# Kernel optimization log

Hardware: AMD Instinct MI355X
Metric: run time of the kernel (lower is better)

## Reference

```python
import jax, jax.numpy as jnp
import numpy as np

# video grid and attention geometry (must match init_kwargs)
F_T, H_T, W_T = 4, 32, 32
K = 3                      # kernel_size (odd)
P = K // 2
T = F_T * H_T * W_T        # max_num_tokens = 4096
HEADS = 8
DIM_HEAD = 64
SCALE = DIM_HEAD ** -0.5
DIM = 512
INNER = HEADS * DIM_HEAD


def _build_window_indices():
    # flat token index grid, padded with sentinel T (out-of-range -> zero row after gather)
    idx = np.arange(T).reshape(F_T, H_T, W_T)
    padded = np.full((F_T + 2 * P, H_T + 2 * P, W_T + 2 * P), T, dtype=np.int64)
    padded[P:P + F_T, P:P + H_T, P:P + W_T] = idx
    # [T, K^3] neighborhood indices, kernel offsets in (kf, kh, kw) C-order (matches unfoldNd)
    win = np.lib.stride_tricks.sliding_window_view(padded, (K, K, K)).reshape(T, K ** 3)
    # causal: mask keys whose flat index is strictly in the future of the query
    causal = np.arange(T)[:, None] < win
    causal = np.concatenate([np.zeros((T, 1), dtype=bool), causal], axis=1)  # BOS column never masked
    return jnp.asarray(win), jnp.asarray(causal)

WIN_IDX, CAUSAL_MASK = _build_window_indices()


def setup_inputs() -> dict:
    key = jax.random.key(0)
    k0, k1, k2, k3 = jax.random.split(key, 4)
    n = T  # 1 BOS + (T-1) video tokens; padding logic pads body to exactly T tokens
    x = jax.random.normal(k0, (2, n, DIM), dtype=jnp.float32)
    Wq = jax.random.normal(k1, (DIM, INNER), dtype=jnp.float32) * (DIM ** -0.5)
    Wkv = jax.random.normal(k2, (DIM, 2 * INNER), dtype=jnp.float32) * (DIM ** -0.5)
    Wo = jax.random.normal(k3, (INNER, DIM), dtype=jnp.float32) * (INNER ** -0.5)
    bo = jnp.zeros((DIM,), dtype=jnp.float32)
    return {"x": x, "Wq": Wq, "Wkv": Wkv, "Wo": Wo, "bo": bo}


def _split_heads(t, b):
    # [b, n, h*d] -> [(b*h), n, d]
    n = t.shape[1]
    return t.reshape(b, n, HEADS, DIM_HEAD).transpose(0, 2, 1, 3).reshape(b * HEADS, n, DIM_HEAD)


def reference(x, Wq, Wkv, Wo, bo):
    b, n, _ = x.shape
    tpf = H_T * W_T
    padding = tpf - (n - 1) % tpf  # pads body tokens to a multiple of tokens_per_frame
    x = jnp.pad(x, ((0, 0), (0, padding), (0, 0)))
    q = x @ Wq
    k, v = jnp.split(x @ Wkv, 2, axis=-1)
    q, k, v = (_split_heads(t, b) for t in (q, k, v))
    bh = b * HEADS
    q = q[:, 1:] * SCALE            # drop BOS query; [bh, T, d]
    bos_v = v[:, :1]                # BOS attends only to itself -> its value passes through
    k_bos, k = k[:, :1], k[:, 1:]
    v_bos, v = v[:, :1], v[:, 1:]
    # gather K^3 3D neighborhoods; sentinel index T maps to a zero row
    zero_row = jnp.zeros((bh, 1, DIM_HEAD), dtype=k.dtype)
    k_nb = jnp.concatenate([k, zero_row], axis=1)[:, WIN_IDX]   # [bh, T, K^3, d]
    v_nb = jnp.concatenate([v, zero_row], axis=1)[:, WIN_IDX]
    # prepend global BOS key/value to every window
    k_nb = jnp.concatenate([jnp.broadcast_to(k_bos[:, :, None], (bh, T, 1, DIM_HEAD)), k_nb], axis=2)
    v_nb = jnp.concatenate([jnp.broadcast_to(v_bos[:, :, None], (bh, T, 1, DIM_HEAD)), v_nb], axis=2)
    sim = jnp.einsum('bid,bijd->bij', q, k_nb)                  # [bh, T, K^3+1]
    sim = jnp.where(CAUSAL_MASK[None], -jnp.finfo(sim.dtype).max, sim)
    attn = jax.nn.softmax(sim, axis=-1)
    out = jnp.einsum('bij,bijd->bid', attn, v_nb)               # [bh, T, d]
    out = jnp.concatenate([bos_v, out], axis=1)                 # [bh, T+1, d]
    np_tok = out.shape[1]
    out = out.reshape(b, HEADS, np_tok, DIM_HEAD).transpose(0, 2, 1, 3).reshape(b, np_tok, INNER)
    return (out @ Wo + bo)[:, :n]
```

## Files before the change

### kernel.cpp

```cpp
#include <hip/hip_runtime.h>


#define T_TOK   4096
#define BATCH   2
#define MROWS   (BATCH * T_TOK)
#define DIM     512
#define NQKV    1536

typedef unsigned short u16;
typedef unsigned int   u32;
typedef unsigned long long u64;
typedef __attribute__((ext_vector_type(8))) short short8;
typedef __attribute__((ext_vector_type(4))) float f32x4;

__device__ __forceinline__ u16 f2bf(float f) {
    u32 u = __float_as_uint(f);
    return (u16)((u + 0x7fffu + ((u >> 16) & 1u)) >> 16);
}
__device__ __forceinline__ float b2f(u16 u) {
    return __uint_as_float(((u32)u) << 16);
}

__device__ __forceinline__ void gload_lds16(const void* g, void* l) {
    __builtin_amdgcn_global_load_lds(
        (const __attribute__((address_space(1))) void*)g,
        (__attribute__((address_space(3))) void*)l, 16, 0, 0);
}

__global__ void cast_all_kernel(const float4* __restrict__ x,
                                const float* __restrict__ Wq, const float* __restrict__ Wkv,
                                const float* __restrict__ Wo,
                                u16* __restrict__ xb, u16* __restrict__ Wt,
                                u16* __restrict__ Wot) {
    int blk = blockIdx.x;
    if (blk < 4096) {
        int i = blk * 256 + threadIdx.x;
        float4 v = x[i];
        u64 pack = (u64)f2bf(v.x) | ((u64)f2bf(v.y) << 16) |
                   ((u64)f2bf(v.z) << 32) | ((u64)f2bf(v.w) << 48);
        ((u64*)xb)[i] = pack;
    } else {
        int idx = (blk - 4096) * 256 + threadIdx.x;
        if (idx < 786432) {
            int k = idx / 1536, n = idx % 1536;
            float v = (n < 512) ? Wq[k * 512 + n] : Wkv[k * 1024 + (n - 512)];
            Wt[n * 512 + k] = f2bf(v);
        } else {
            int i2 = idx - 786432;
            int k = i2 >> 9, n = i2 & 511;
            Wot[n * 512 + k] = f2bf(Wo[k * 512 + n]);
        }
    }
}

template <int MODE>
__global__ __launch_bounds__(256)
void gemm_nt(const u16* __restrict__ A, const u16* __restrict__ B,
             void* __restrict__ Cv, const float* __restrict__ bias,
             int lda, int ldb, int ldc) {
    constexpr int K = 512, BK = 32;
    __shared__ __align__(16) char lds[16384];
    const int tid  = threadIdx.x;
    const int lane = tid & 63, wave = tid >> 6;
    const int quad = lane >> 4, mrow = lane & 15;
    const int wm = wave >> 1, wn = wave & 1;
    const int bm = blockIdx.y, bn = blockIdx.x;

    const char* gptr[4];
    char*       lptr[4];
    #pragma unroll
    for (int it = 0; it < 4; ++it) {
        int c   = it * 256 + tid;
        int inB = (c >= 512);
        int a   = inB ? c - 512 : c;
        int r   = a >> 2;
        int kc  = ((a & 3) - (r >> 1)) & 3;
        int row = (inB ? bn : bm) * 128 + r;
        const u16* base = inB ? B : A;
        int ld = inB ? ldb : lda;
        gptr[it] = (const char*)(base + (size_t)row * ld + kc * 8);
        lptr[it] = (char*)lds + it * 4096 + wave * 1024;
    }
    const short8* aLds[4];
    const short8* bLds[4];
    #pragma unroll
    for (int i = 0; i < 4; ++i) {
        int ra = wm * 64 + i * 16 + mrow;
        aLds[i] = (const short8*)(lds + (ra * 4 + ((quad + (ra >> 1)) & 3)) * 16);
        int rb = wn * 64 + i * 16 + mrow;
        bLds[i] = (const short8*)(lds + 8192 + (rb * 4 + ((quad + (rb >> 1)) & 3)) * 16);
    }

    f32x4 acc[4][4] = {};
    for (int k0 = 0; k0 < K; k0 += BK) {
        #pragma unroll
        for (int it = 0; it < 4; ++it)
            gload_lds16(gptr[it] + 2 * k0, lptr[it]);
        __syncthreads();
        short8 af[4], bf[4];
        #pragma unroll
        for (int i = 0; i < 4; ++i) { af[i] = *aLds[i]; bf[i] = *bLds[i]; }
        #pragma unroll
        for (int i = 0; i < 4; ++i)
            #pragma unroll
            for (int j = 0; j < 4; ++j)
                acc[i][j] = __builtin_amdgcn_mfma_f32_16x16x32_bf16(af[i], bf[j], acc[i][j], 0, 0, 0);
        __syncthreads();
    }

    #pragma unroll
    for (int i = 0; i < 4; ++i) {
        #pragma unroll
        for (int j = 0; j < 4; ++j) {
            int colg = bn * 128 + wn * 64 + j * 16 + mrow;
            #pragma unroll
            for (int r = 0; r < 4; ++r) {
                int rowg = bm * 128 + wm * 64 + i * 16 + quad * 4 + r;
                if (MODE == 0) {
                    ((u16*)Cv)[(size_t)rowg * ldc + colg] = f2bf(acc[i][j][r]);
                } else {
                    ((float*)Cv)[(size_t)rowg * ldc + colg] = acc[i][j][r] + bias[colg];
                }
            }
        }
    }
}

__global__ __launch_bounds__(256)
void attn_kernel(const u16* __restrict__ QKV, u16* __restrict__ O) {
    const int wid  = blockIdx.x * 4 + (threadIdx.x >> 6);
    const int lane = threadIdx.x & 63;
    const int bh = wid >> 12;
    const int ti = wid & 4095;
    const int b = bh >> 3, h = bh & 7;
    const size_t baseQ = (size_t)b * T_TOK * NQKV;
    const size_t baseO = (size_t)b * T_TOK * DIM;

    if (ti == 0) {
        O[baseO + h * 64 + lane] = QKV[baseQ + 1024 + h * 64 + lane];
        return;
    }
    const int t = ti - 1;
    const int f = t >> 10, hh = (t >> 5) & 31, ww = t & 31;

    const int j = lane >> 2, g = lane & 3;
    int jm1 = j - 1;
    int dh9 = ((jm1 * 11) >> 5) - 1;
    int dw9 = jm1 - (dh9 + 1) * 3 - 1;
    int df = (j >= 1 && j <= 9) ? -1 : 0;
    int dh = (j >= 1 && j <= 9) ? dh9 : ((j >= 10 && j <= 12) ? -1 : 0);
    int dw = (j >= 1 && j <= 9) ? dw9 :
             ((j >= 10 && j <= 12) ? (j - 11) : ((j == 13) ? -1 : 0));
    int nf = f + df, nh = hh + dh, nw = ww + dw;
    int valid = (nf >= 0) && ((unsigned)nh < 32u) && ((unsigned)nw < 32u)
                && (j >= 1) && (j <= 14);
    int p = valid ? (t + 1 + df * 1024 + dh * 32 + dw) : 0;
    int score_on = valid || (j == 0);

    const u16* qrow = QKV + baseQ + (size_t)(t + 1) * NQKV + h * 64 + g * 16;
    short8 q0 = *(const short8*)qrow;
    short8 q1 = *(const short8*)(qrow + 8);
    const u16* krow = QKV + baseQ + (size_t)p * NQKV + 512 + h * 64 + g * 16;
    short8 k0 = *(const short8*)krow;
    short8 k1 = *(const short8*)(krow + 8);
    float s = 0.f;
    #pragma unroll
    for (int i = 0; i < 8; ++i) {
        s += b2f((u16)q0[i]) * b2f((u16)k0[i]);
        s += b2f((u16)q1[i]) * b2f((u16)k1[i]);
    }
    s += __shfl_xor(s, 1);
    s += __shfl_xor(s, 2);
    s *= 0.125f;
    s = score_on ? s : -3.0e38f;

    float m = s;
    #pragma unroll
    for (int off = 4; off <= 32; off <<= 1) m = fmaxf(m, __shfl_xor(m, off));
    float pe = __expf(s - m);
    float l = pe;
    #pragma unroll
    for (int off = 4; off <= 32; off <<= 1) l += __shfl_xor(l, off);

    float acc = 0.f;
    const u16* vbase = QKV + baseQ + 1024 + h * 64 + lane;
    #pragma unroll
    for (int jj = 0; jj < 15; ++jj) {
        int   ps = __builtin_amdgcn_readlane(p, jj * 4);
        float pj = __uint_as_float(
                     (u32)__builtin_amdgcn_readlane((int)__float_as_uint(pe), jj * 4));
        float vv = b2f(vbase[(size_t)ps * NQKV]);
        acc += pj * vv;
    }
    O[baseO + (size_t)ti * DIM + h * 64 + lane] = f2bf(acc * __frcp_rn(l));
}

extern "C" void kernel_launch(void* const* d_in, const int* in_sizes, int n_in,
                              void* d_out, int out_size, void* d_ws, size_t ws_size,
                              hipStream_t stream) {
    const float* x   = (const float*)d_in[0];
    const float* Wq  = (const float*)d_in[1];
    const float* Wkv = (const float*)d_in[2];
    const float* Wo  = (const float*)d_in[3];
    const float* bo  = (const float*)d_in[4];
    float* out = (float*)d_out;
    char* ws = (char*)d_ws;

    u16* xb  = (u16*)(ws + 0);
    u16* Wt  = (u16*)(ws + 8388608);
    u16* Wot = (u16*)(ws + 9961472);
    u16* QKV = (u16*)(ws + 10485760);
    u16* O   = (u16*)(ws + 0);

    cast_all_kernel<<<dim3(8192), dim3(256), 0, stream>>>(
        (const float4*)x, Wq, Wkv, Wo, xb, Wt, Wot);
    gemm_nt<0><<<dim3(12, 64), dim3(256), 0, stream>>>(xb, Wt, (void*)QKV, nullptr, 512, 512, 1536);
    attn_kernel<<<dim3(16384), dim3(256), 0, stream>>>(QKV, O);
    gemm_nt<1><<<dim3(4, 64), dim3(256), 0, stream>>>(O, Wot, (void*)out, bo, 512, 512, 512);
}
```

Baseline: 142.2 us.

## Tile weight transposes through LDS, retile output GEMM, streamline attention gather

Result: slower. 147.9 us (+4.0%).

```diff
diff --git a/kernel.cpp b/kernel.cpp
--- a/kernel.cpp
+++ b/kernel.cpp
@@ -2,8 +2,6 @@
 
 
 #define T_TOK   4096
-#define BATCH   2
-#define MROWS   (BATCH * T_TOK)
 #define DIM     512
 #define NQKV    1536
 
@@ -32,90 +30,112 @@
                                 const float* __restrict__ Wo,
                                 u16* __restrict__ xb, u16* __restrict__ Wt,
                                 u16* __restrict__ Wot) {
+    __shared__ float S[64 * 65];
     int blk = blockIdx.x;
+    int tid = threadIdx.x;
     if (blk < 4096) {
-        int i = blk * 256 + threadIdx.x;
+        int i = blk * 256 + tid;
         float4 v = x[i];
         u64 pack = (u64)f2bf(v.x) | ((u64)f2bf(v.y) << 16) |
                    ((u64)f2bf(v.z) << 32) | ((u64)f2bf(v.w) << 48);
         ((u64*)xb)[i] = pack;
-    } else {
-        int idx = (blk - 4096) * 256 + threadIdx.x;
-        if (idx < 786432) {
-            int k = idx / 1536, n = idx % 1536;
-            float v = (n < 512) ? Wq[k * 512 + n] : Wkv[k * 1024 + (n - 512)];
-            Wt[n * 512 + k] = f2bf(v);
-        } else {
-            int i2 = idx - 786432;
-            int k = i2 >> 9, n = i2 & 511;
-            Wot[n * 512 + k] = f2bf(Wo[k * 512 + n]);
-        }
-    }
-}
-
-template <int MODE>
+        return;
+    }
+    int isWo = blk >= 4288;
+    int tIdx = isWo ? (blk - 4288) : (blk - 4096);
+    int tn = tIdx >> 3, tk = tIdx & 7;
+    #pragma unroll
+    for (int p = 0; p < 16; ++p) {
+        int kl = p * 4 + (tid >> 6), nl = tid & 63;
+        int gk = tk * 64 + kl, gn = tn * 64 + nl;
+        float v;
+        if (isWo)            v = Wo[gk * 512 + gn];
+        else if (gn < 512)   v = Wq[gk * 512 + gn];
+        else                 v = Wkv[gk * 1024 + (gn - 512)];
+        S[kl * 65 + nl] = v;
+    }
+    __syncthreads();
+    u16* dst = isWo ? Wot : Wt;
+    #pragma unroll
+    for (int p = 0; p < 16; ++p) {
+        int nl = p * 4 + (tid >> 6), kl = tid & 63;
+        dst[(size_t)(tn * 64 + nl) * 512 + tk * 64 + kl] = f2bf(S[kl * 65 + nl]);
+    }
+}
+
+template <int BM, int BN, int MODE>
 __global__ __launch_bounds__(256)
 void gemm_nt(const u16* __restrict__ A, const u16* __restrict__ B,
              void* __restrict__ Cv, const float* __restrict__ bias,
              int lda, int ldb, int ldc) {
     constexpr int K = 512, BK = 32;
-    __shared__ __align__(16) char lds[16384];
+    constexpr int ACH = BM * 4;
+    constexpr int NCH = (BM + BN) * 4;
+    constexpr int NLD = NCH / 256;
+    constexpr int ABYTES = BM * 64;
+    constexpr int MI = BM / 32, NJ = BN / 32;
+    __shared__ __align__(16) char lds[(BM + BN) * 64];
     const int tid  = threadIdx.x;
     const int lane = tid & 63, wave = tid >> 6;
     const int quad = lane >> 4, mrow = lane & 15;
     const int wm = wave >> 1, wn = wave & 1;
     const int bm = blockIdx.y, bn = blockIdx.x;
 
-    const char* gptr[4];
-    char*       lptr[4];
-    #pragma unroll
-    for (int it = 0; it < 4; ++it) {
+    const char* gptr[NLD];
+    char*       lptr[NLD];
+    #pragma unroll
+    for (int it = 0; it < NLD; ++it) {
         int c   = it * 256 + tid;
-        int inB = (c >= 512);
-        int a   = inB ? c - 512 : c;
+        int inB = (c >= ACH);
+        int a   = inB ? c - ACH : c;
         int r   = a >> 2;
         int kc  = ((a & 3) - (r >> 1)) & 3;
-        int row = (inB ? bn : bm) * 128 + r;
+        int row = (inB ? bn * BN : bm * BM) + r;
         const u16* base = inB ? B : A;
         int ld = inB ? ldb : lda;
         gptr[it] = (const char*)(base + (size_t)row * ld + kc * 8);
-        lptr[it] = (char*)lds + it * 4096 + wave * 1024;
-    }
-    const short8* aLds[4];
-    const short8* bLds[4];
-    #pragma unroll
-    for (int i = 0; i < 4; ++i) {
-        int ra = wm * 64 + i * 16 + mrow;
+        lptr[it] = (char*)lds + (it * 256 + wave * 64) * 16;
+    }
+    const short8* aLds[MI];
+    const short8* bLds[NJ];
+    #pragma unroll
+    for (int i = 0; i < MI; ++i) {
+        int ra = wm * (BM / 2) + i * 16 + mrow;
         aLds[i] = (const short8*)(lds + (ra * 4 + ((quad + (ra >> 1)) & 3)) * 16);
-        int rb = wn * 64 + i * 16 + mrow;
-        bLds[i] = (const short8*)(lds + 8192 + (rb * 4 + ((quad + (rb >> 1)) & 3)) * 16);
-    }
-
-    f32x4 acc[4][4] = {};
+    }
+    #pragma unroll
+    for (int j = 0; j < NJ; ++j) {
+        int rb = wn * (BN / 2) + j * 16 + mrow;
+        bLds[j] = (const short8*)(lds + ABYTES + (rb * 4 + ((quad + (rb >> 1)) & 3)) * 16);
+    }
+
+    f32x4 acc[MI][NJ] = {};
     for (int k0 = 0; k0 < K; k0 += BK) {
         #pragma unroll
-        for (int it = 0; it < 4; ++it)
+        for (int it = 0; it < NLD; ++it)
             gload_lds16(gptr[it] + 2 * k0, lptr[it]);
         __syncthreads();
-        short8 af[4], bf[4];
-        #pragma unroll
-        for (int i = 0; i < 4; ++i) { af[i] = *aLds[i]; bf[i] = *bLds[i]; }
-        #pragma unroll
-        for (int i = 0; i < 4; ++i)
+        short8 af[MI], bf[NJ];
+        #pragma unroll
+        for (int i = 0; i < MI; ++i) af[i] = *aLds[i];
+        #pragma unroll
+        for (int j = 0; j < NJ; ++j) bf[j] = *bLds[j];
+        #pragma unroll
+        for (int i = 0; i < MI; ++i)
             #pragma unroll
-            for (int j = 0; j < 4; ++j)
+            for (int j = 0; j < NJ; ++j)
                 acc[i][j] = __builtin_amdgcn_mfma_f32_16x16x32_bf16(af[i], bf[j], acc[i][j], 0, 0, 0);
         __syncthreads();
     }
 
     #pragma unroll
-    for (int i = 0; i < 4; ++i) {
-        #pragma unroll
-        for (int j = 0; j < 4; ++j) {
-            int colg = bn * 128 + wn * 64 + j * 16 + mrow;
+    for (int i = 0; i < MI; ++i) {
+        #pragma unroll
+        for (int j = 0; j < NJ; ++j) {
+            int colg = bn * BN + wn * (BN / 2) + j * 16 + mrow;
             #pragma unroll
             for (int r = 0; r < 4; ++r) {
-                int rowg = bm * 128 + wm * 64 + i * 16 + quad * 4 + r;
+                int rowg = bm * BM + wm * (BM / 2) + i * 16 + quad * 4 + r;
                 if (MODE == 0) {
                     ((u16*)Cv)[(size_t)rowg * ldc + colg] = f2bf(acc[i][j][r]);
                 } else {
@@ -166,8 +186,8 @@
     float s = 0.f;
     #pragma unroll
     for (int i = 0; i < 8; ++i) {
-        s += b2f((u16)q0[i]) * b2f((u16)k0[i]);
-        s += b2f((u16)q1[i]) * b2f((u16)k1[i]);
+        s = fmaf(b2f((u16)q0[i]), b2f((u16)k0[i]), s);
+        s = fmaf(b2f((u16)q1[i]), b2f((u16)k1[i]), s);
     }
     s += __shfl_xor(s, 1);
     s += __shfl_xor(s, 2);
@@ -181,18 +201,20 @@
     float l = pe;
     #pragma unroll
     for (int off = 4; off <= 32; off <<= 1) l += __shfl_xor(l, off);
+    float pen = pe * __frcp_rn(l);
+    u32 voff = (u32)p * 3072u;
 
     float acc = 0.f;
-    const u16* vbase = QKV + baseQ + 1024 + h * 64 + lane;
+    const char* vb = (const char*)(QKV + baseQ + 1024 + h * 64 + lane);
     #pragma unroll
     for (int jj = 0; jj < 15; ++jj) {
-        int   ps = __builtin_amdgcn_readlane(p, jj * 4);
+        u32 o = (u32)__builtin_amdgcn_readlane((int)voff, jj * 4);
         float pj = __uint_as_float(
-                     (u32)__builtin_amdgcn_readlane((int)__float_as_uint(pe), jj * 4));
-        float vv = b2f(vbase[(size_t)ps * NQKV]);
-        acc += pj * vv;
-    }
-    O[baseO + (size_t)ti * DIM + h * 64 + lane] = f2bf(acc * __frcp_rn(l));
+                     (u32)__builtin_amdgcn_readlane((int)__float_as_uint(pen), jj * 4));
+        float vv = b2f(*(const u16*)(vb + o));
+        acc = fmaf(pj, vv, acc);
+    }
+    O[baseO + (size_t)ti * DIM + h * 64 + lane] = f2bf(acc);
 }
 
 extern "C" void kernel_launch(void* const* d_in, const int* in_sizes, int n_in,
@@ -212,9 +234,11 @@
     u16* QKV = (u16*)(ws + 10485760);
     u16* O   = (u16*)(ws + 0);
 
-    cast_all_kernel<<<dim3(8192), dim3(256), 0, stream>>>(
+    cast_all_kernel<<<dim3(4352), dim3(256), 0, stream>>>(
         (const float4*)x, Wq, Wkv, Wo, xb, Wt, Wot);
-    gemm_nt<0><<<dim3(12, 64), dim3(256), 0, stream>>>(xb, Wt, (void*)QKV, nullptr, 512, 512, 1536);
+    gemm_nt<128, 128, 0><<<dim3(12, 64), dim3(256), 0, stream>>>(
+        xb, Wt, (void*)QKV, nullptr, 512, 512, 1536);
     attn_kernel<<<dim3(16384), dim3(256), 0, stream>>>(QKV, O);
-    gemm_nt<1><<<dim3(4, 64), dim3(256), 0, stream>>>(O, Wot, (void*)out, bo, 512, 512, 512);
-}
+    gemm_nt<128, 64, 1><<<dim3(8, 64), dim3(256), 0, stream>>>(
+        O, Wot, (void*)out, bo, 512, 512, 512);
+}
```
